# Optimization experiments

Hardware: AMD Instinct MI355X
Metric: run time of the kernel (lower is better)

## Reference

```python
import jax, jax.numpy as jnp
import numpy as np

EPS = 1e-5

def _dw_conv_bn(x, w, gamma, beta):
    # depthwise 'same' conv: w is (C,1,k,k), feature_group_count = C
    C = x.shape[1]
    k = w.shape[-1]
    p = k // 2
    y = jax.lax.conv_general_dilated(
        x, w,
        window_strides=(1, 1),
        padding=((p, p), (p, p)),
        dimension_numbers=("NCHW", "OIHW", "NCHW"),
        feature_group_count=C,
    )
    # BatchNorm2d (training mode: batch stats over N,H,W per channel, biased var)
    mean = jnp.mean(y, axis=(0, 2, 3), keepdims=True)
    var = jnp.var(y, axis=(0, 2, 3), keepdims=True)
    inv = jax.lax.rsqrt(var + EPS)
    g = gamma.reshape(1, -1, 1, 1)
    b = beta.reshape(1, -1, 1, 1)
    return (y - mean) * inv * g + b


def setup_inputs() -> dict:
    key = jax.random.key(0)
    ks = jax.random.split(key, 3)
    B, C, H, W = 16, 384, 56, 56
    x = jax.random.normal(ks[0], (B, C, H, W), dtype=jnp.float32)
    w_large = jax.random.normal(ks[1], (C, 1, 31, 31), dtype=jnp.float32) * 0.02
    w_small = jax.random.normal(ks[2], (C, 1, 5, 5), dtype=jnp.float32) * 0.1
    gamma_large = jnp.ones((C,), dtype=jnp.float32)
    beta_large = jnp.zeros((C,), dtype=jnp.float32)
    gamma_small = jnp.ones((C,), dtype=jnp.float32)
    beta_small = jnp.zeros((C,), dtype=jnp.float32)
    return {
        "x": x,
        "w_large": w_large, "gamma_large": gamma_large, "beta_large": beta_large,
        "w_small": w_small, "gamma_small": gamma_small, "beta_small": beta_small,
    }


def reference(x, w_large, gamma_large, beta_large, w_small, gamma_small, beta_small):
    out = _dw_conv_bn(x, w_large, gamma_large, beta_large)
    out = out + _dw_conv_bn(x, w_small, gamma_small, beta_small)
    return out
```

## Files before the change

### kernel.cpp

```cpp
#include <hip/hip_runtime.h>
#include <hip/hip_bf16.h>

#define BB 16
#define CC 384
#define HH 56
#define WW 56
#define PLANE (HH*WW)
#define NHW (BB*PLANE)

typedef __attribute__((ext_vector_type(8)))  short short8;
typedef __attribute__((ext_vector_type(16))) float f32x16;
typedef unsigned int uint;

#define PSTR 92
#define PROWS 86
#define PSZ (PROWS*PSTR)
#define WL_W 100
#define WS_W 80

static __device__ __forceinline__ short f2bf(float f) {
    unsigned int u = __float_as_uint(f);
    unsigned int r = (u + 0x7fffu + ((u >> 16) & 1u)) >> 16;
    return (short)r;
}

static __device__ __forceinline__ short8 ldA(const short* ap) {
    union { uint u[4]; short8 v; } r;
    uint2 lo = *(const uint2*)(ap);
    uint2 hi = *(const uint2*)(ap + 4);
    r.u[0] = lo.x; r.u[1] = lo.y; r.u[2] = hi.x; r.u[3] = hi.y;
    return r.v;
}

static __device__ __forceinline__ short8 ldW(const uint* p) {
    union { uint u[4]; short8 v; } r;
    r.u[0] = p[0]; r.u[1] = p[2]; r.u[2] = p[4]; r.u[3] = p[6];
    return r.v;
}

template<bool PACK>
__global__ __launch_bounds__(256)
__attribute__((amdgpu_waves_per_eu(3)))
void conv_large_k(
    const float* __restrict__ x, const float* __restrict__ wL,
    const float* __restrict__ wS,
    unsigned short* __restrict__ yL, uint* __restrict__ pk,
    float* __restrict__ stats)
{
    __shared__ __align__(16) short planes[2*PSZ];
    __shared__ __align__(16) uint  wpL[31*WL_W];
    __shared__ __align__(16) uint  wpS[5*WS_W];
    __shared__ float red_s[16];

    const int bid  = blockIdx.x;
    const int c    = bid % CC;
    const int pg   = bid / CC;
    const int tid  = threadIdx.x;
    const int w    = tid >> 6;
    const int p    = w >> 1;
    const int tx   = w & 1;
    const int lane = tid & 63;
    const int m    = lane & 31;
    const int g    = lane >> 5;

    {
        uint4 z = make_uint4(0,0,0,0);
        uint4* p4 = (uint4*)planes;
        #pragma unroll 1
        for (int i = tid; i < 2*PSZ/8; i += 256) p4[i] = z;
    }
    __syncthreads();

    short* pl = planes + p*PSZ;
    const int b = pg*2 + p;
    const float4* xp4 = (const float4*)(x + ((size_t)b*CC + c)*PLANE);
    #pragma unroll 1
    for (int i4 = lane + 64*tx; i4 < PLANE/4; i4 += 128) {
        float4 v = xp4[i4];
        int e  = 4*i4;
        int r  = e / WW;
        int cc = e - r*WW;
        short* dst = &pl[(r + 15)*PSTR + cc + 15];
        dst[0] = f2bf(v.x); dst[1] = f2bf(v.y); dst[2] = f2bf(v.z); dst[3] = f2bf(v.w);
    }

    const float* wrow = wL + c*961;
    #pragma unroll 1
    for (int i = tid; i < 31*WL_W; i += 256) {
        int ky = i / WL_W;
        int j  = i - ky*WL_W;
        int widx = j - 32;
        uint lo = (widx   >= 0 && widx   < 31) ? (uint)(unsigned short)f2bf(wrow[ky*31 + widx])     : 0u;
        uint hi = (widx+1 >= 0 && widx+1 < 31) ? (uint)(unsigned short)f2bf(wrow[ky*31 + widx + 1]) : 0u;
        wpL[i] = lo | (hi << 16);
    }
    const float* wrowS = wS + c*25;
    #pragma unroll 1
    for (int i = tid; i < 5*WS_W; i += 256) {
        int ky = i / WS_W;
        int j  = i - ky*WS_W;
        int widx = j - 32;
        uint lo = (widx   >= 0 && widx   < 5) ? (uint)(unsigned short)f2bf(wrowS[ky*5 + widx])     : 0u;
        uint hi = (widx+1 >= 0 && widx+1 < 5) ? (uint)(unsigned short)f2bf(wrowS[ky*5 + widx + 1]) : 0u;
        wpS[i] = lo | (hi << 16);
    }
    __syncthreads();

    const int  toff = 8*g - m;
    const uint* wLd = wpL + (toff + 32);
    const uint* wSd = wpS + (toff + 31);
    const short* abase = pl + m*PSTR + 8*g + tx*24;

    f32x16 acc[2] = {};

    #pragma unroll 1
    for (int ky = 0; ky < 31; ++ky) {
        const uint* wk = wLd + ky*WL_W;
        short8 Bv[4];
        #pragma unroll
        for (int s = 0; s < 4; ++s) Bv[s] = ldW(wk + 16*s);
        const short* ar = abase + ky*PSTR;
        #pragma unroll
        for (int s = 0; s < 4; ++s) {
            short8 A0 = ldA(ar + 16*s);
            short8 A1 = ldA(ar + 24*PSTR + 16*s);
            acc[0] = __builtin_amdgcn_mfma_f32_32x32x16_bf16(A0, Bv[s], acc[0], 0, 0, 0);
            acc[1] = __builtin_amdgcn_mfma_f32_32x32x16_bf16(A1, Bv[s], acc[1], 0, 0, 0);
        }
    }

    float sL = 0.f, sL2 = 0.f, sS = 0.f, sS2 = 0.f;
    unsigned short* yout = yL + ((size_t)b*CC + c)*PLANE;
    uint*           pout = pk + ((size_t)b*CC + c)*PLANE;

    #pragma unroll
    for (int ty = 0; ty < 2; ++ty) {
        __builtin_amdgcn_sched_barrier(0);
        f32x16 aS_ = {};
        const short* asb = abase + (ty*24 + 13)*PSTR + 12;
        #pragma unroll 1
        for (int k2 = 0; k2 < 5; ++k2) {
            const uint* wk2 = wSd + k2*WS_W;
            const short* ar2 = asb + k2*PSTR;
            #pragma unroll
            for (int s = 0; s < 3; ++s) {
                short8 bs = ldW(wk2 + 16*s);
                short8 av = ldA(ar2 + 16*s);
                aS_ = __builtin_amdgcn_mfma_f32_32x32x16_bf16(av, bs, aS_, 0, 0, 0);
            }
        }
        const float cm = (tx == 0 || m >= 8) ? 1.f : 0.f;
        #pragma unroll
        for (int r = 0; r < 16; ++r) {
            float v  = acc[ty][r];
            float v2 = aS_[r];
            if (ty == 0 || r >= 4) {
                sL  = fmaf(cm, v,   sL);
                sL2 = fmaf(cm, v*v, sL2);
                sS  = fmaf(cm, v2,    sS);
                sS2 = fmaf(cm, v2*v2, sS2);
            }
            const int row = (r & 3) + 8*(r >> 2) + 4*g;
            const int ofs = (ty*24 + row)*WW + tx*24 + m;
            if (PACK) {
                pout[ofs] = (uint)(unsigned short)f2bf(v) | ((uint)(unsigned short)f2bf(v2) << 16);
            } else {
                yout[ofs] = (unsigned short)f2bf(v);
            }
        }
    }

    #pragma unroll
    for (int off = 32; off > 0; off >>= 1) {
        sL  += __shfl_down(sL,  off);
        sL2 += __shfl_down(sL2, off);
        sS  += __shfl_down(sS,  off);
        sS2 += __shfl_down(sS2, off);
    }
    if (lane == 0) {
        red_s[w*4 + 0] = sL;  red_s[w*4 + 1] = sL2;
        red_s[w*4 + 2] = sS;  red_s[w*4 + 3] = sS2;
    }
    __syncthreads();
    if (tid == 0) {
        float a = 0.f, e = 0.f, d0 = 0.f, e2 = 0.f;
        #pragma unroll
        for (int i = 0; i < 4; ++i) {
            a  += red_s[i*4 + 0]; e  += red_s[i*4 + 1];
            d0 += red_s[i*4 + 2]; e2 += red_s[i*4 + 3];
        }
        atomicAdd(&stats[c],        a);
        atomicAdd(&stats[CC + c],   e);
        atomicAdd(&stats[2*CC + c], d0);
        atomicAdd(&stats[3*CC + c], e2);
    }
}

__global__ __launch_bounds__(256) void fuse_pack_k(
    const uint* __restrict__ pk, const float* __restrict__ stats,
    const float* __restrict__ gL, const float* __restrict__ bL,
    const float* __restrict__ gS, const float* __restrict__ bS,
    float* __restrict__ out)
{
    const int bid = blockIdx.x;
    const int c   = bid % CC;
    const int tid = threadIdx.x;

    const uint4* pp = (const uint4*)(pk + (size_t)bid * PLANE);
    float4*      op = (float4*)(out + (size_t)bid * PLANE);

    uint4 v0 = pp[tid];
    uint4 v1 = pp[tid + 256];
    uint4 v2 = pp[tid + 512];

    const float inv_n = 1.0f / (float)NHW;
    float mL = stats[c]          * inv_n;
    float vL = stats[CC + c]     * inv_n - mL * mL;
    float aL = rsqrtf(vL + 1e-5f) * gL[c];
    float mS = stats[2*CC + c]   * inv_n;
    float vS = stats[3*CC + c]   * inv_n - mS * mS;
    float aS = rsqrtf(vS + 1e-5f) * gS[c];
    float cst = bL[c] + bS[c] - mL * aL - mS * aS;

    #define AFF(u) fmaf(aL, __uint_as_float((u) << 16), fmaf(aS, __uint_as_float((u) & 0xffff0000u), cst))
    float4 r0, r1, r2;
    r0.x = AFF(v0.x); r0.y = AFF(v0.y); r0.z = AFF(v0.z); r0.w = AFF(v0.w);
    r1.x = AFF(v1.x); r1.y = AFF(v1.y); r1.z = AFF(v1.z); r1.w = AFF(v1.w);
    r2.x = AFF(v2.x); r2.y = AFF(v2.y); r2.z = AFF(v2.z); r2.w = AFF(v2.w);
    op[tid]       = r0;
    op[tid + 256] = r1;
    op[tid + 512] = r2;
    if (tid < PLANE/4 - 768) {
        uint4 v3 = pp[tid + 768];
        float4 r3;
        r3.x = AFF(v3.x); r3.y = AFF(v3.y); r3.z = AFF(v3.z); r3.w = AFF(v3.w);
        op[tid + 768] = r3;
    }
    #undef AFF
}

#define ST3 61
__global__ __launch_bounds__(256) void fuse_small_k(
    const float* __restrict__ x, const float* __restrict__ wS,
    const unsigned short* __restrict__ yL, const float* __restrict__ stats,
    const float* __restrict__ gL, const float* __restrict__ bL,
    const float* __restrict__ gS, const float* __restrict__ bS,
    float* __restrict__ out)
{
    __shared__ float in_s[60 * ST3];

    const int bid = blockIdx.x;
    const int c   = bid % CC;
    const int tid = threadIdx.x;
    const float* __restrict__ w2 = wS + c * 25;

    for (int i = tid; i < 60 * ST3; i += 256) in_s[i] = 0.f;
    __syncthreads();

    const float4* xp4 = (const float4*)(x + (size_t)bid * PLANE);
    for (int t = tid; t < PLANE / 4; t += 256) {
        int r  = t / (WW / 4);
        int c4 = (t - r * (WW / 4)) * 4;
        float4 v = xp4[t];
        float* dst = &in_s[(r + 2) * ST3 + 2 + c4];
        dst[0] = v.x; dst[1] = v.y; dst[2] = v.z; dst[3] = v.w;
    }
    __syncthreads();

    const float inv_n = 1.0f / (float)NHW;
    float mL = stats[c]          * inv_n;
    float vL = stats[CC + c]     * inv_n - mL * mL;
    float aL = rsqrtf(vL + 1e-5f) * gL[c];
    float mS = stats[2*CC + c]   * inv_n;
    float vS = stats[3*CC + c]   * inv_n - mS * mS;
    float aS = rsqrtf(vS + 1e-5f) * gS[c];
    float cst = bL[c] + bS[c] - mL * aL - mS * aS;

    const unsigned short* yp = yL + (size_t)bid * PLANE;
    float* op = out + (size_t)bid * PLANE;

    #pragma unroll 1
    for (int t = tid; t < PLANE / 4; t += 256) {
        int r  = t / 14;
        int c4 = (t - r * 14) * 4;
        float o0 = 0.f, o1 = 0.f, o2 = 0.f, o3 = 0.f;
        #pragma unroll
        for (int ky = 0; ky < 5; ++ky) {
            const float* rp = &in_s[(r + ky) * ST3 + c4];
            float f[9];
            #pragma unroll
            for (int j = 0; j < 9; ++j) f[j] = rp[j];
            const float* wr = w2 + ky * 5;
            #pragma unroll
            for (int kx = 0; kx < 5; ++kx) {
                float wv = wr[kx];
                o0 = fmaf(f[kx + 0], wv, o0);
                o1 = fmaf(f[kx + 1], wv, o1);
                o2 = fmaf(f[kx + 2], wv, o2);
                o3 = fmaf(f[kx + 3], wv, o3);
            }
        }
        ushort4 yv = *(const ushort4*)(yp + 4 * t);
        float4 res;
        res.x = fmaf(aL, __uint_as_float(((uint)yv.x) << 16), fmaf(aS, o0, cst));
        res.y = fmaf(aL, __uint_as_float(((uint)yv.y) << 16), fmaf(aS, o1, cst));
        res.z = fmaf(aL, __uint_as_float(((uint)yv.z) << 16), fmaf(aS, o2, cst));
        res.w = fmaf(aL, __uint_as_float(((uint)yv.w) << 16), fmaf(aS, o3, cst));
        *(float4*)(op + 4 * t) = res;
    }
}

extern "C" void kernel_launch(void* const* d_in, const int* in_sizes, int n_in,
                              void* d_out, int out_size, void* d_ws, size_t ws_size,
                              hipStream_t stream) {
    const float* x  = (const float*)d_in[0];
    const float* wL = (const float*)d_in[1];
    const float* gL = (const float*)d_in[2];
    const float* bL = (const float*)d_in[3];
    const float* wS = (const float*)d_in[4];
    const float* gS = (const float*)d_in[5];
    const float* bS = (const float*)d_in[6];
    float* out = (float*)d_out;

    const size_t pk_bytes = (size_t)BB * CC * PLANE * sizeof(uint);
    const size_t yl_bytes = (size_t)BB * CC * PLANE * sizeof(unsigned short);
    const bool pack = ws_size >= pk_bytes + 4 * CC * sizeof(float);

    if (pack) {
        uint* pkbuf  = (uint*)d_ws;
        float* stats = (float*)((char*)d_ws + pk_bytes);
        hipMemsetAsync(stats, 0, 4 * CC * sizeof(float), stream);
        conv_large_k<true><<<8 * CC, 256, 0, stream>>>(x, wL, wS, (unsigned short*)d_ws, pkbuf, stats);
        fuse_pack_k<<<BB * CC, 256, 0, stream>>>(pkbuf, stats, gL, bL, gS, bS, out);
    } else {
        unsigned short* yLbuf = (unsigned short*)d_ws;
        float* stats = (float*)((char*)d_ws + yl_bytes);
        hipMemsetAsync(stats, 0, 4 * CC * sizeof(float), stream);
        conv_large_k<false><<<8 * CC, 256, 0, stream>>>(x, wL, wS, yLbuf, (uint*)d_ws, stats);
        fuse_small_k<<<BB * CC, 256, 0, stream>>>(x, wS, yLbuf, stats, gL, bL, gS, bS, out);
    }
}
```

Measured before the change: 279.9 us.

## Software-pipeline large conv ky loop and widen fuse kernel with nontemporal accesses

The 31-tap row loop of the large depthwise conv now double-buffers A and B fragments, so the LDS loads for row ky+1 are issued before the MFMAs for row ky. This is meant to hide LDS latency behind matrix work, at the cost of more live VGPRs. The fuse/pack kernel now handles two planes per block (grid halved; bid+3072 keeps the same channel) and uses nontemporal loads and stores to avoid polluting the cache with streaming data.

```diff
diff --git a/kernel.cpp b/kernel.cpp
--- a/kernel.cpp
+++ b/kernel.cpp
@@ -10,6 +10,8 @@
 
 typedef __attribute__((ext_vector_type(8)))  short short8;
 typedef __attribute__((ext_vector_type(16))) float f32x16;
+typedef __attribute__((ext_vector_type(4)))  unsigned int uint4v;
+typedef __attribute__((ext_vector_type(4)))  float float4v;
 typedef unsigned int uint;
 
 #define PSTR 92
@@ -113,20 +115,55 @@
 
     f32x16 acc[2] = {};
 
-    #pragma unroll 1
-    for (int ky = 0; ky < 31; ++ky) {
-        const uint* wk = wLd + ky*WL_W;
-        short8 Bv[4];
-        #pragma unroll
-        for (int s = 0; s < 4; ++s) Bv[s] = ldW(wk + 16*s);
-        const short* ar = abase + ky*PSTR;
+    short8 A0[8], B0[4], A1[8], B1[4];
+    {
+        #pragma unroll
+        for (int s = 0; s < 4; ++s) B0[s] = ldW(wLd + 16*s);
         #pragma unroll
         for (int s = 0; s < 4; ++s) {
-            short8 A0 = ldA(ar + 16*s);
-            short8 A1 = ldA(ar + 24*PSTR + 16*s);
-            acc[0] = __builtin_amdgcn_mfma_f32_32x32x16_bf16(A0, Bv[s], acc[0], 0, 0, 0);
-            acc[1] = __builtin_amdgcn_mfma_f32_32x32x16_bf16(A1, Bv[s], acc[1], 0, 0, 0);
-        }
+            A0[2*s]   = ldA(abase + 16*s);
+            A0[2*s+1] = ldA(abase + 24*PSTR + 16*s);
+        }
+    }
+    #pragma unroll 1
+    for (int ky = 0; ky < 30; ky += 2) {
+        {
+            const uint* wk = wLd + (ky+1)*WL_W;
+            const short* ar = abase + (ky+1)*PSTR;
+            #pragma unroll
+            for (int s = 0; s < 4; ++s) B1[s] = ldW(wk + 16*s);
+            #pragma unroll
+            for (int s = 0; s < 4; ++s) {
+                A1[2*s]   = ldA(ar + 16*s);
+                A1[2*s+1] = ldA(ar + 24*PSTR + 16*s);
+            }
+            #pragma unroll
+            for (int s = 0; s < 4; ++s) {
+                acc[0] = __builtin_amdgcn_mfma_f32_32x32x16_bf16(A0[2*s],   B0[s], acc[0], 0, 0, 0);
+                acc[1] = __builtin_amdgcn_mfma_f32_32x32x16_bf16(A0[2*s+1], B0[s], acc[1], 0, 0, 0);
+            }
+        }
+        {
+            const uint* wk = wLd + (ky+2)*WL_W;
+            const short* ar = abase + (ky+2)*PSTR;
+            #pragma unroll
+            for (int s = 0; s < 4; ++s) B0[s] = ldW(wk + 16*s);
+            #pragma unroll
+            for (int s = 0; s < 4; ++s) {
+                A0[2*s]   = ldA(ar + 16*s);
+                A0[2*s+1] = ldA(ar + 24*PSTR + 16*s);
+            }
+            #pragma unroll
+            for (int s = 0; s < 4; ++s) {
+                acc[0] = __builtin_amdgcn_mfma_f32_32x32x16_bf16(A1[2*s],   B1[s], acc[0], 0, 0, 0);
+                acc[1] = __builtin_amdgcn_mfma_f32_32x32x16_bf16(A1[2*s+1], B1[s], acc[1], 0, 0, 0);
+            }
+        }
+    }
+    #pragma unroll
+    for (int s = 0; s < 4; ++s) {
+        acc[0] = __builtin_amdgcn_mfma_f32_32x32x16_bf16(A0[2*s],   B0[s], acc[0], 0, 0, 0);
+        acc[1] = __builtin_amdgcn_mfma_f32_32x32x16_bf16(A0[2*s+1], B0[s], acc[1], 0, 0, 0);
     }
 
     float sL = 0.f, sL2 = 0.f, sS = 0.f, sS2 = 0.f;
@@ -206,12 +243,17 @@
     const int c   = bid % CC;
     const int tid = threadIdx.x;
 
-    const uint4* pp = (const uint4*)(pk + (size_t)bid * PLANE);
-    float4*      op = (float4*)(out + (size_t)bid * PLANE);
-
-    uint4 v0 = pp[tid];
-    uint4 v1 = pp[tid + 256];
-    uint4 v2 = pp[tid + 512];
+    const uint4v* pp0 = (const uint4v*)(pk + (size_t)bid * PLANE);
+    const uint4v* pp1 = (const uint4v*)(pk + ((size_t)bid + 3072) * PLANE);
+    float4v* op0 = (float4v*)(out + (size_t)bid * PLANE);
+    float4v* op1 = (float4v*)(out + ((size_t)bid + 3072) * PLANE);
+
+    uint4v v0 = __builtin_nontemporal_load(pp0 + tid);
+    uint4v v1 = __builtin_nontemporal_load(pp0 + tid + 256);
+    uint4v v2 = __builtin_nontemporal_load(pp0 + tid + 512);
+    uint4v v3 = __builtin_nontemporal_load(pp1 + tid);
+    uint4v v4 = __builtin_nontemporal_load(pp1 + tid + 256);
+    uint4v v5 = __builtin_nontemporal_load(pp1 + tid + 512);
 
     const float inv_n = 1.0f / (float)NHW;
     float mL = stats[c]          * inv_n;
@@ -223,19 +265,21 @@
     float cst = bL[c] + bS[c] - mL * aL - mS * aS;
 
     #define AFF(u) fmaf(aL, __uint_as_float((u) << 16), fmaf(aS, __uint_as_float((u) & 0xffff0000u), cst))
-    float4 r0, r1, r2;
-    r0.x = AFF(v0.x); r0.y = AFF(v0.y); r0.z = AFF(v0.z); r0.w = AFF(v0.w);
-    r1.x = AFF(v1.x); r1.y = AFF(v1.y); r1.z = AFF(v1.z); r1.w = AFF(v1.w);
-    r2.x = AFF(v2.x); r2.y = AFF(v2.y); r2.z = AFF(v2.z); r2.w = AFF(v2.w);
-    op[tid]       = r0;
-    op[tid + 256] = r1;
-    op[tid + 512] = r2;
+    #define AFF4(dst, src) { float4v t_; t_[0]=AFF(src[0]); t_[1]=AFF(src[1]); t_[2]=AFF(src[2]); t_[3]=AFF(src[3]); dst = t_; }
+    float4v r;
+    AFF4(r, v0); __builtin_nontemporal_store(r, op0 + tid);
+    AFF4(r, v1); __builtin_nontemporal_store(r, op0 + tid + 256);
+    AFF4(r, v2); __builtin_nontemporal_store(r, op0 + tid + 512);
+    AFF4(r, v3); __builtin_nontemporal_store(r, op1 + tid);
+    AFF4(r, v4); __builtin_nontemporal_store(r, op1 + tid + 256);
+    AFF4(r, v5); __builtin_nontemporal_store(r, op1 + tid + 512);
     if (tid < PLANE/4 - 768) {
-        uint4 v3 = pp[tid + 768];
-        float4 r3;
-        r3.x = AFF(v3.x); r3.y = AFF(v3.y); r3.z = AFF(v3.z); r3.w = AFF(v3.w);
-        op[tid + 768] = r3;
-    }
+        uint4v t0 = __builtin_nontemporal_load(pp0 + tid + 768);
+        uint4v t1 = __builtin_nontemporal_load(pp1 + tid + 768);
+        AFF4(r, t0); __builtin_nontemporal_store(r, op0 + tid + 768);
+        AFF4(r, t1); __builtin_nontemporal_store(r, op1 + tid + 768);
+    }
+    #undef AFF4
     #undef AFF
 }
 
@@ -331,7 +375,7 @@
         float* stats = (float*)((char*)d_ws + pk_bytes);
         hipMemsetAsync(stats, 0, 4 * CC * sizeof(float), stream);
         conv_large_k<true><<<8 * CC, 256, 0, stream>>>(x, wL, wS, (unsigned short*)d_ws, pkbuf, stats);
-        fuse_pack_k<<<BB * CC, 256, 0, stream>>>(pkbuf, stats, gL, bL, gS, bS, out);
+        fuse_pack_k<<<BB * CC / 2, 256, 0, stream>>>(pkbuf, stats, gL, bL, gS, bS, out);
     } else {
         unsigned short* yLbuf = (unsigned short*)d_ws;
         float* stats = (float*)((char*)d_ws + yl_bytes);
```

New measurement: 273.9 us. 2.1% less time.
